# Kernel optimization log

Measured on AMD Instinct MI355X. Metric: run time of the kernel, lower is better.

Reference implementation:

```python
import jax, jax.numpy as jnp
import numpy as np

# Fixed multi-scale pyramid (H, W) per level -- static config, closed over.
SPATIAL_SHAPES = [(100, 100), (50, 50), (25, 25), (13, 13)]
D_MODEL, N_HEADS, N_LEVELS, N_POINTS = 256, 8, 4, 4
C_HEAD = D_MODEL // N_HEADS
B = 2
NUM_KEYS = sum(h * w for h, w in SPATIAL_SHAPES)  # 13294
NUM_QUERIES = NUM_KEYS


def setup_inputs() -> dict:
    key = jax.random.key(0)
    ks = jax.random.split(key, 12)
    d = D_MODEL
    return {
        "query": jax.random.normal(ks[0], (B, NUM_QUERIES, d), jnp.float32),
        "reference_points": jax.random.uniform(ks[1], (B, NUM_QUERIES, N_LEVELS, 2), jnp.float32),
        "input_flatten": jax.random.normal(ks[2], (B, NUM_KEYS, d), jnp.float32),
        "Wv": jax.random.normal(ks[3], (d, d), jnp.float32) * 0.02,
        "bv": jnp.zeros((d,), jnp.float32),
        "Ws": jax.random.normal(ks[4], (d, N_HEADS * N_LEVELS * N_POINTS * 2), jnp.float32) * 0.01,
        "bs": jax.random.normal(ks[5], (N_HEADS * N_LEVELS * N_POINTS * 2,), jnp.float32),
        "Wa": jax.random.normal(ks[6], (d, N_HEADS * N_LEVELS * N_POINTS), jnp.float32) * 0.02,
        "ba": jnp.zeros((N_HEADS * N_LEVELS * N_POINTS,), jnp.float32),
        "Wo": jax.random.normal(ks[7], (d, d), jnp.float32) * 0.02,
        "bo": jnp.zeros((d,), jnp.float32),
    }


def _bilinear_sample(v, grid, H, W):
    """torch.F.grid_sample(mode='bilinear', padding_mode='zeros', align_corners=False).
    v: (N, H, W, C); grid: (N, M, 2) with (x, y) in [-1, 1]. Returns (N, M, C)."""
    x = (grid[..., 0] + 1.0) * (W * 0.5) - 0.5
    y = (grid[..., 1] + 1.0) * (H * 0.5) - 0.5
    x0 = jnp.floor(x)
    y0 = jnp.floor(y)
    dx = x - x0
    dy = y - y0
    x0i = x0.astype(jnp.int32)
    y0i = y0.astype(jnp.int32)
    vflat = v.reshape(v.shape[0], H * W, v.shape[-1])

    def gather(xi, yi):
        valid = (xi >= 0) & (xi < W) & (yi >= 0) & (yi < H)
        idx = jnp.clip(yi, 0, H - 1) * W + jnp.clip(xi, 0, W - 1)  # (N, M)
        g = jnp.take_along_axis(vflat, idx[..., None], axis=1)
        return g * valid[..., None]

    v00 = gather(x0i, y0i)
    v10 = gather(x0i + 1, y0i)
    v01 = gather(x0i, y0i + 1)
    v11 = gather(x0i + 1, y0i + 1)
    return (v00 * ((1 - dx) * (1 - dy))[..., None]
            + v10 * (dx * (1 - dy))[..., None]
            + v01 * ((1 - dx) * dy)[..., None]
            + v11 * (dx * dy)[..., None])


def _ms_deform_attn(value, sampling_locations, attention_weights):
    # value: (B, NK, H, Ch); loc: (B, NQ, H, L, P, 2); w: (B, NQ, H, L, P)
    grids = 2.0 * sampling_locations - 1.0
    splits = np.cumsum([h * w for h, w in SPATIAL_SHAPES])[:-1]
    value_list = jnp.split(value, splits, axis=1)
    acc = 0.0
    for lvl, (H, W) in enumerate(SPATIAL_SHAPES):
        # (B, H*W, heads, Ch) -> (B*heads, H, W, Ch)
        v_l = value_list[lvl].reshape(B, H, W, N_HEADS, C_HEAD)
        v_l = v_l.transpose(0, 3, 1, 2, 4).reshape(B * N_HEADS, H, W, C_HEAD)
        # (B, NQ, heads, P, 2) -> (B*heads, NQ*P, 2)
        g_l = grids[:, :, :, lvl].transpose(0, 2, 1, 3, 4).reshape(B * N_HEADS, -1, 2)
        samp = _bilinear_sample(v_l, g_l, H, W)  # (B*heads, NQ*P, Ch)
        samp = samp.reshape(B, N_HEADS, -1, N_POINTS, C_HEAD)
        w_l = attention_weights[:, :, :, lvl].transpose(0, 2, 1, 3)  # (B, heads, NQ, P)
        acc = acc + jnp.einsum("bhqpc,bhqp->bhqc", samp, w_l)
    return acc.transpose(0, 2, 1, 3).reshape(B, -1, D_MODEL)  # (B, NQ, d_model)


def reference(query, reference_points, input_flatten, Wv, bv, Ws, bs, Wa, ba, Wo, bo):
    value = (input_flatten @ Wv + bv).reshape(B, NUM_KEYS, N_HEADS, C_HEAD)
    offsets = (query @ Ws + bs).reshape(B, NUM_QUERIES, N_HEADS, N_LEVELS, N_POINTS, 2)
    attw = jax.nn.softmax(
        (query @ Wa + ba).reshape(B, NUM_QUERIES, N_HEADS, N_LEVELS * N_POINTS), axis=-1
    ).reshape(B, NUM_QUERIES, N_HEADS, N_LEVELS, N_POINTS)
    # NOTE: module divides by [H, W] (not [W, H]) -- replicated faithfully.
    normalizer = jnp.asarray(SPATIAL_SHAPES, jnp.float32)  # (L, 2) = (H, W)
    normalizer = jnp.clip(normalizer, 1.0)
    loc = reference_points[:, :, None, :, None, :] + offsets / normalizer[None, None, None, :, None, :]
    out = _ms_deform_attn(value, loc, attw)
    return out @ Wo + bo
```

## Files before the change

kernel.cpp:

```cpp
#include <hip/hip_runtime.h>
#include <hip/hip_bf16.h>
#include <math.h>

#define B_  2
#define NQ  13294
#define NK  13294
#define M_  (B_ * NK)
#define MT  32
#define GX  ((M_ + MT - 1) / MT)

typedef __bf16 bf16x8 __attribute__((ext_vector_type(8)));
typedef float f32x4 __attribute__((ext_vector_type(4)));

static __device__ __forceinline__ f32x4 mfma16(bf16x8 a, bf16x8 b, f32x4 c) {
  return __builtin_amdgcn_mfma_f32_16x16x32_bf16(a, b, c, 0, 0, 0);
}

static __device__ __forceinline__ void pack_one(
    const float* __restrict__ W1, const float* __restrict__ W2,
    int N1, int Ntot, __hip_bfloat16* __restrict__ out, int g) {
  int lane = g & 63;
  int n_sub = (g >> 6) & 3;
  int kt = (g >> 8) & 7;
  int bn = g >> 11;
  int n = bn * 64 + n_sub * 16 + (lane & 15);
  int k0 = kt * 32 + (lane >> 4) * 8;
  const float* src; int nn, Ns;
  if (n < N1) { src = W1; nn = n; Ns = N1; }
  else        { src = W2; nn = n - N1; Ns = Ntot - N1; }
  bf16x8 v;
#pragma unroll
  for (int j = 0; j < 8; ++j) v[j] = (__bf16)src[(size_t)(k0 + j) * Ns + nn];
  *(bf16x8*)(out + (size_t)g * 8) = v;
}

__global__ __launch_bounds__(256) void pack_all(
    const float* __restrict__ Wv, const float* __restrict__ Ws,
    const float* __restrict__ Wa, const float* __restrict__ Wo,
    __hip_bfloat16* __restrict__ wv_p, __hip_bfloat16* __restrict__ wsa_p,
    __hip_bfloat16* __restrict__ wo_p) {
  const int b = blockIdx.x, t = threadIdx.x;
  if (b < 32)       pack_one(Wv, Wv, 256, 256, wv_p,  b * 256 + t);
  else if (b < 80)  pack_one(Ws, Wa, 256, 384, wsa_p, (b - 32) * 256 + t);
  else              pack_one(Wo, Wo, 256, 256, wo_p,  (b - 80) * 256 + t);
}

#define CSTR 68

__global__ __launch_bounds__(128) void gemm_mt(
    const float* __restrict__ inpf, const float* __restrict__ query,
    const __hip_bfloat16* __restrict__ accin,
    const bf16x8* __restrict__ wv_p, const bf16x8* __restrict__ wsa_p,
    const bf16x8* __restrict__ wo_p,
    const float* __restrict__ bv, const float* __restrict__ bs,
    const float* __restrict__ ba, const float* __restrict__ bo,
    __hip_bfloat16* __restrict__ value, float* __restrict__ params,
    float* __restrict__ outp, int mode_base) {
  __shared__ bf16x8 As[8 * 2 * 64];
  __shared__ float  Cs[2 * MT * CSTR];

  const int t = threadIdx.x;
  const int bm = blockIdx.x * MT;
  const int lane = t & 63, wid = t >> 6;
  const int mode = mode_base + blockIdx.y;

  {
    const int r = t >> 2;
    const int row = bm + r;
    const int sm = r >> 4;
    const int lb = r & 15;
    const bool ok = row < M_;
    if (mode != 2) {
      const float* Af = (mode == 0) ? inpf : query;
      const float* ap = Af + (size_t)row * 256 + (t & 3) * 64;
#pragma unroll
      for (int gi = 0; gi < 8; ++gi) {
        float4 u = make_float4(0.f,0.f,0.f,0.f), v = make_float4(0.f,0.f,0.f,0.f);
        if (ok) { u = *(const float4*)(ap + gi * 8); v = *(const float4*)(ap + gi * 8 + 4); }
        bf16x8 w;
        w[0]=(__bf16)u.x; w[1]=(__bf16)u.y; w[2]=(__bf16)u.z; w[3]=(__bf16)u.w;
        w[4]=(__bf16)v.x; w[5]=(__bf16)v.y; w[6]=(__bf16)v.z; w[7]=(__bf16)v.w;
        int k8 = (t & 3) * 8 + gi;
        As[((k8 >> 2) * 2 + sm) * 64 + lb + ((k8 & 3) << 4)] = w;
      }
    } else {
      const __hip_bfloat16* ap = accin + (size_t)row * 256 + (t & 3) * 64;
#pragma unroll
      for (int gi = 0; gi < 8; ++gi) {
        bf16x8 w = {};
        if (ok) w = *(const bf16x8*)(ap + gi * 8);
        int k8 = (t & 3) * 8 + gi;
        As[((k8 >> 2) * 2 + sm) * 64 + lb + ((k8 & 3) << 4)] = w;
      }
    }
  }
  __syncthreads();

  const bf16x8* Bp = (mode == 0) ? wv_p : (mode == 1) ? wsa_p : wo_p;
  const int NB = (mode == 1) ? 6 : 4;
  float* Cw = &Cs[wid * MT * CSTR];

  for (int nb = wid; nb < NB; nb += 2) {
    const int colbase = nb * 64;
    const bf16x8* bpn = Bp + (size_t)nb * 2048;

    f32x4 acc[2][4] = {};
#pragma unroll
    for (int kt = 0; kt < 8; ++kt) {
      bf16x8 a0 = As[(kt * 2 + 0) * 64 + lane];
      bf16x8 a1 = As[(kt * 2 + 1) * 64 + lane];
#pragma unroll
      for (int n = 0; n < 4; ++n) {
        bf16x8 b = bpn[(kt * 4 + n) * 64 + lane];
        acc[0][n] = mfma16(a0, b, acc[0][n]);
        acc[1][n] = mfma16(a1, b, acc[1][n]);
      }
    }

#pragma unroll
    for (int m = 0; m < 2; ++m)
#pragma unroll
      for (int n = 0; n < 4; ++n)
#pragma unroll
        for (int rg = 0; rg < 4; ++rg)
          Cw[(m * 16 + (lane >> 4) * 4 + rg) * CSTR + n * 16 + (lane & 15)] = acc[m][n][rg];

    if (mode == 0) {
#pragma unroll
      for (int p = 0; p < 4; ++p) {
        const int r = (lane >> 3) + p * 8;
        const int c = (lane & 7) * 8;
        const int row = bm + r;
        float4 u = *(float4*)&Cw[r * CSTR + c];
        float4 v = *(float4*)&Cw[r * CSTR + c + 4];
        const float* bias = bv + colbase + c;
        bf16x8 o;
        o[0]=(__bf16)(u.x+bias[0]); o[1]=(__bf16)(u.y+bias[1]);
        o[2]=(__bf16)(u.z+bias[2]); o[3]=(__bf16)(u.w+bias[3]);
        o[4]=(__bf16)(v.x+bias[4]); o[5]=(__bf16)(v.y+bias[5]);
        o[6]=(__bf16)(v.z+bias[6]); o[7]=(__bf16)(v.w+bias[7]);
        if (row < M_)
          *(bf16x8*)(value + (size_t)row * 256 + colbase + c) = o;
      }
    } else {
      float* Of = (mode == 1) ? params : outp;
      const int stride = (mode == 1) ? 384 : 256;
#pragma unroll
      for (int p = 0; p < 8; ++p) {
        const int r = (lane >> 4) + p * 4;
        const int c = (lane & 15) * 4;
        const int row = bm + r;
        const int col = colbase + c;
        float4 u = *(float4*)&Cw[r * CSTR + c];
        const float* bias;
        if (mode == 1) bias = (col < 256) ? (bs + col) : (ba + col - 256);
        else           bias = bo + col;
        u.x += bias[0]; u.y += bias[1]; u.z += bias[2]; u.w += bias[3];
        if (row < M_)
          *(float4*)(Of + (size_t)row * stride + col) = u;
      }
    }
  }
}

#define CS 65

__global__ __launch_bounds__(256) void sampler(
    const float* __restrict__ refp, const float* __restrict__ params,
    const __hip_bfloat16* __restrict__ value, __hip_bfloat16* __restrict__ acc_out) {
  __shared__ unsigned int combo[64 * CS];

  const int t = threadIdx.x;
  const int q0 = blockIdx.x * 16;
  const int bb = blockIdx.y;

  const int cqi = t >> 5;
  const int chh = (t >> 2) & 7;
  const int cl  = t & 3;

  const int lane = t & 63;
  const int wid  = t >> 6;
  const int q2   = lane >> 5;
  const int gh   = (lane >> 2) & 7;
  const int gs   = lane & 3;
  const char* vb = (const char*)value;
  const unsigned int voff0 = (unsigned int)bb * (NK * 512u) + (unsigned)(gh * 64 + gs * 16);

  const float DIMF[4]  = {100.f, 50.f, 25.f, 13.f};
  const int   LSTART[4] = {0, 10000, 12500, 13125};
  const float dimf  = DIMF[cl];
  const int   Wd    = (int)dimf;
  const int   lbase = LSTART[cl];

  for (int qc = 0; qc < 16; qc += 8) {
    __syncthreads();
    {
      const int q = q0 + qc + cqi;
      const bool valid = q < NQ;
      const size_t row = (size_t)bb * NQ + (valid ? q : 0);
      const float* pr = params + row * 384;
      const float* lg = pr + 256 + chh * 16;
      float m = lg[0];
#pragma unroll
      for (int j = 1; j < 16; ++j) m = fmaxf(m, lg[j]);
      float s = 0.f;
#pragma unroll
      for (int j = 0; j < 16; ++j) s += __expf(lg[j] - m);
      const float inv = valid ? 1.f / s : 0.f;

      const float rx = refp[(row * 4 + cl) * 2 + 0];
      const float ry = refp[(row * 4 + cl) * 2 + 1];
      const float* of = pr + chh * 32 + cl * 8;
      unsigned int* cb = &combo[(cqi * 8 + chh) * CS + cl * 16];

#pragma unroll
      for (int p = 0; p < 4; ++p) {
        const float wa = __expf(lg[cl * 4 + p] - m) * inv;
        const float x = rx * dimf + of[p * 2 + 0] - 0.5f;
        const float y = ry * dimf + of[p * 2 + 1] - 0.5f;
        const float xf = floorf(x), yf = floorf(y);
        const float dx = x - xf, dy = y - yf;
        const int x0 = (int)xf, y0 = (int)yf;
        float w00 = (1.f - dx) * (1.f - dy) * wa;
        float w10 = dx * (1.f - dy) * wa;
        float w01 = (1.f - dx) * dy * wa;
        float w11 = dx * dy * wa;
        int i0, i1, i2, i3, xi, yi;
        xi = x0;     yi = y0;
        if (xi >= 0 && xi < Wd && yi >= 0 && yi < Wd) i0 = lbase + yi * Wd + xi; else { i0 = 0; w00 = 0.f; }
        xi = x0 + 1; yi = y0;
        if (xi >= 0 && xi < Wd && yi >= 0 && yi < Wd) i1 = lbase + yi * Wd + xi; else { i1 = 0; w10 = 0.f; }
        xi = x0;     yi = y0 + 1;
        if (xi >= 0 && xi < Wd && yi >= 0 && yi < Wd) i2 = lbase + yi * Wd + xi; else { i2 = 0; w01 = 0.f; }
        xi = x0 + 1; yi = y0 + 1;
        if (xi >= 0 && xi < Wd && yi >= 0 && yi < Wd) i3 = lbase + yi * Wd + xi; else { i3 = 0; w11 = 0.f; }
        cb[p * 4 + 0] = ((__float_as_uint(w00) + 0x8000u) & 0xffff0000u) | (unsigned)i0;
        cb[p * 4 + 1] = ((__float_as_uint(w10) + 0x8000u) & 0xffff0000u) | (unsigned)i1;
        cb[p * 4 + 2] = ((__float_as_uint(w01) + 0x8000u) & 0xffff0000u) | (unsigned)i2;
        cb[p * 4 + 3] = ((__float_as_uint(w11) + 0x8000u) & 0xffff0000u) | (unsigned)i3;
      }
    }
    __syncthreads();

    {
      const int qw = wid * 2 + q2;
      const int q = q0 + qc + qw;
      const unsigned int* cb = &combo[(qw * 8 + gh) * CS];
      float a0=0.f,a1=0.f,a2=0.f,a3=0.f,a4=0.f,a5=0.f,a6=0.f,a7=0.f;
#pragma unroll 16
      for (int e = 0; e < 64; ++e) {
        const unsigned int u = cb[e];
        const float w = __uint_as_float(u & 0xffff0000u);
        const unsigned int voff = voff0 + ((u & 0xffffu) << 9);
        const uint4 v = *(const uint4*)(vb + (size_t)voff);
        a0 += w * __uint_as_float(v.x << 16);
        a1 += w * __uint_as_float(v.x & 0xffff0000u);
        a2 += w * __uint_as_float(v.y << 16);
        a3 += w * __uint_as_float(v.y & 0xffff0000u);
        a4 += w * __uint_as_float(v.z << 16);
        a5 += w * __uint_as_float(v.z & 0xffff0000u);
        a6 += w * __uint_as_float(v.w << 16);
        a7 += w * __uint_as_float(v.w & 0xffff0000u);
      }
      if (q < NQ) {
        bf16x8 o;
        o[0]=(__bf16)a0; o[1]=(__bf16)a1; o[2]=(__bf16)a2; o[3]=(__bf16)a3;
        o[4]=(__bf16)a4; o[5]=(__bf16)a5; o[6]=(__bf16)a6; o[7]=(__bf16)a7;
        *(bf16x8*)((char*)acc_out + (((size_t)bb * NQ + q) * 256 + gh * 32 + gs * 8) * 2) = o;
      }
    }
  }
}

extern "C" void kernel_launch(void* const* d_in, const int* in_sizes, int n_in,
                              void* d_out, int out_size, void* d_ws, size_t ws_size,
                              hipStream_t stream) {
  const float* query = (const float*)d_in[0];
  const float* refp  = (const float*)d_in[1];
  const float* inpf  = (const float*)d_in[2];
  const float* Wv    = (const float*)d_in[3];
  const float* bv    = (const float*)d_in[4];
  const float* Ws    = (const float*)d_in[5];
  const float* bs    = (const float*)d_in[6];
  const float* Wa    = (const float*)d_in[7];
  const float* ba    = (const float*)d_in[8];
  const float* Wo    = (const float*)d_in[9];
  const float* bo    = (const float*)d_in[10];
  float* out = (float*)d_out;

  char* w = (char*)d_ws;
  __hip_bfloat16* value  = (__hip_bfloat16*)w;            w += (size_t)M_ * 256 * 2;
  __hip_bfloat16* acc    = (__hip_bfloat16*)w;            w += (size_t)M_ * 256 * 2;
  float*          params = (float*)w;                     w += (size_t)M_ * 384 * 4;
  __hip_bfloat16* wv_p   = (__hip_bfloat16*)w;            w += 256 * 256 * 2;
  __hip_bfloat16* wsa_p  = (__hip_bfloat16*)w;            w += 256 * 384 * 2;
  __hip_bfloat16* wo_p   = (__hip_bfloat16*)w;

  pack_all<<<112, 256, 0, stream>>>(Wv, Ws, Wa, Wo, wv_p, wsa_p, wo_p);

  gemm_mt<<<dim3(GX, 2), 128, 0, stream>>>(
      inpf, query, acc, (const bf16x8*)wv_p, (const bf16x8*)wsa_p,
      (const bf16x8*)wo_p, bv, bs, ba, bo, value, params, out, 0);

  dim3 sgrid((NQ + 15) / 16, B_);
  sampler<<<sgrid, 256, 0, stream>>>(refp, params, value, acc);

  gemm_mt<<<dim3(GX, 1), 128, 0, stream>>>(
      inpf, query, acc, (const bf16x8*)wv_p, (const bf16x8*)wsa_p,
      (const bf16x8*)wo_p, bv, bs, ba, bo, value, params, out, 2);
}
```

Measured before the change: 141.2 us.

## Enlarge GEMM row tile to 64 with 4 waves; double-buffer sampler LDS

```diff
diff --git a/kernel.cpp b/kernel.cpp
--- a/kernel.cpp
+++ b/kernel.cpp
@@ -6,7 +6,7 @@
 #define NQ  13294
 #define NK  13294
 #define M_  (B_ * NK)
-#define MT  32
+#define MT  64
 #define GX  ((M_ + MT - 1) / MT)
 
 typedef __bf16 bf16x8 __attribute__((ext_vector_type(8)));
@@ -47,7 +47,7 @@
 
 #define CSTR 68
 
-__global__ __launch_bounds__(128) void gemm_mt(
+__global__ __launch_bounds__(256) void gemm_mt(
     const float* __restrict__ inpf, const float* __restrict__ query,
     const __hip_bfloat16* __restrict__ accin,
     const bf16x8* __restrict__ wv_p, const bf16x8* __restrict__ wsa_p,
@@ -56,8 +56,8 @@
     const float* __restrict__ ba, const float* __restrict__ bo,
     __hip_bfloat16* __restrict__ value, float* __restrict__ params,
     float* __restrict__ outp, int mode_base) {
-  __shared__ bf16x8 As[8 * 2 * 64];
-  __shared__ float  Cs[2 * MT * CSTR];
+  __shared__ bf16x8 As[8 * 4 * 64];
+  __shared__ float  Cs[4 * 16 * CSTR];
 
   const int t = threadIdx.x;
   const int bm = blockIdx.x * MT;
@@ -81,7 +81,7 @@
         w[0]=(__bf16)u.x; w[1]=(__bf16)u.y; w[2]=(__bf16)u.z; w[3]=(__bf16)u.w;
         w[4]=(__bf16)v.x; w[5]=(__bf16)v.y; w[6]=(__bf16)v.z; w[7]=(__bf16)v.w;
         int k8 = (t & 3) * 8 + gi;
-        As[((k8 >> 2) * 2 + sm) * 64 + lb + ((k8 & 3) << 4)] = w;
+        As[((k8 >> 2) * 4 + sm) * 64 + lb + ((k8 & 3) << 4)] = w;
       }
     } else {
       const __hip_bfloat16* ap = accin + (size_t)row * 256 + (t & 3) * 64;
@@ -90,7 +90,7 @@
         bf16x8 w = {};
         if (ok) w = *(const bf16x8*)(ap + gi * 8);
         int k8 = (t & 3) * 8 + gi;
-        As[((k8 >> 2) * 2 + sm) * 64 + lb + ((k8 & 3) << 4)] = w;
+        As[((k8 >> 2) * 4 + sm) * 64 + lb + ((k8 & 3) << 4)] = w;
       }
     }
   }
@@ -98,66 +98,73 @@
 
   const bf16x8* Bp = (mode == 0) ? wv_p : (mode == 1) ? wsa_p : wo_p;
   const int NB = (mode == 1) ? 6 : 4;
-  float* Cw = &Cs[wid * MT * CSTR];
-
-  for (int nb = wid; nb < NB; nb += 2) {
+  float* Cw = &Cs[wid * 16 * CSTR];
+
+  for (int nb = wid; nb < NB; nb += 4) {
     const int colbase = nb * 64;
     const bf16x8* bpn = Bp + (size_t)nb * 2048;
 
-    f32x4 acc[2][4] = {};
+    f32x4 acc[4][4] = {};
 #pragma unroll
     for (int kt = 0; kt < 8; ++kt) {
-      bf16x8 a0 = As[(kt * 2 + 0) * 64 + lane];
-      bf16x8 a1 = As[(kt * 2 + 1) * 64 + lane];
+      bf16x8 a0 = As[(kt * 4 + 0) * 64 + lane];
+      bf16x8 a1 = As[(kt * 4 + 1) * 64 + lane];
+      bf16x8 a2 = As[(kt * 4 + 2) * 64 + lane];
+      bf16x8 a3 = As[(kt * 4 + 3) * 64 + lane];
 #pragma unroll
       for (int n = 0; n < 4; ++n) {
         bf16x8 b = bpn[(kt * 4 + n) * 64 + lane];
         acc[0][n] = mfma16(a0, b, acc[0][n]);
         acc[1][n] = mfma16(a1, b, acc[1][n]);
-      }
-    }
-
-#pragma unroll
-    for (int m = 0; m < 2; ++m)
+        acc[2][n] = mfma16(a2, b, acc[2][n]);
+        acc[3][n] = mfma16(a3, b, acc[3][n]);
+      }
+    }
+
+#pragma unroll
+    for (int m = 0; m < 4; ++m) {
 #pragma unroll
       for (int n = 0; n < 4; ++n)
 #pragma unroll
         for (int rg = 0; rg < 4; ++rg)
-          Cw[(m * 16 + (lane >> 4) * 4 + rg) * CSTR + n * 16 + (lane & 15)] = acc[m][n][rg];
-
-    if (mode == 0) {
-#pragma unroll
-      for (int p = 0; p < 4; ++p) {
-        const int r = (lane >> 3) + p * 8;
-        const int c = (lane & 7) * 8;
-        const int row = bm + r;
-        float4 u = *(float4*)&Cw[r * CSTR + c];
-        float4 v = *(float4*)&Cw[r * CSTR + c + 4];
-        const float* bias = bv + colbase + c;
-        bf16x8 o;
-        o[0]=(__bf16)(u.x+bias[0]); o[1]=(__bf16)(u.y+bias[1]);
-        o[2]=(__bf16)(u.z+bias[2]); o[3]=(__bf16)(u.w+bias[3]);
-        o[4]=(__bf16)(v.x+bias[4]); o[5]=(__bf16)(v.y+bias[5]);
-        o[6]=(__bf16)(v.z+bias[6]); o[7]=(__bf16)(v.w+bias[7]);
-        if (row < M_)
-          *(bf16x8*)(value + (size_t)row * 256 + colbase + c) = o;
-      }
-    } else {
-      float* Of = (mode == 1) ? params : outp;
-      const int stride = (mode == 1) ? 384 : 256;
-#pragma unroll
-      for (int p = 0; p < 8; ++p) {
-        const int r = (lane >> 4) + p * 4;
-        const int c = (lane & 15) * 4;
-        const int row = bm + r;
-        const int col = colbase + c;
-        float4 u = *(float4*)&Cw[r * CSTR + c];
-        const float* bias;
-        if (mode == 1) bias = (col < 256) ? (bs + col) : (ba + col - 256);
-        else           bias = bo + col;
-        u.x += bias[0]; u.y += bias[1]; u.z += bias[2]; u.w += bias[3];
-        if (row < M_)
-          *(float4*)(Of + (size_t)row * stride + col) = u;
+          Cw[((lane >> 4) * 4 + rg) * CSTR + n * 16 + (lane & 15)] = acc[m][n][rg];
+
+      const int lr = lane >> 2;
+      const int c0 = (lane & 3) * 16;
+      const int row = bm + m * 16 + lr;
+      const int col = colbase + c0;
+      float vv[16];
+      *(float4*)&vv[0]  = *(float4*)&Cw[lr * CSTR + c0 + 0];
+      *(float4*)&vv[4]  = *(float4*)&Cw[lr * CSTR + c0 + 4];
+      *(float4*)&vv[8]  = *(float4*)&Cw[lr * CSTR + c0 + 8];
+      *(float4*)&vv[12] = *(float4*)&Cw[lr * CSTR + c0 + 12];
+
+      if (mode == 0) {
+        const float* bias = bv + col;
+        bf16x8 o0, o1;
+#pragma unroll
+        for (int j = 0; j < 8; ++j) {
+          o0[j] = (__bf16)(vv[j] + bias[j]);
+          o1[j] = (__bf16)(vv[8 + j] + bias[8 + j]);
+        }
+        if (row < M_) {
+          *(bf16x8*)(value + (size_t)row * 256 + col + 0) = o0;
+          *(bf16x8*)(value + (size_t)row * 256 + col + 8) = o1;
+        }
+      } else {
+        float* Of = (mode == 1) ? params : outp;
+        const int stride = (mode == 1) ? 384 : 256;
+        const float* bias = (mode == 2) ? (bo + col)
+                          : (col < 256 ? bs + col : ba + col - 256);
+#pragma unroll
+        for (int j = 0; j < 16; ++j) vv[j] += bias[j];
+        if (row < M_) {
+          float* dst = Of + (size_t)row * stride + col;
+          *(float4*)(dst + 0)  = *(float4*)&vv[0];
+          *(float4*)(dst + 4)  = *(float4*)&vv[4];
+          *(float4*)(dst + 8)  = *(float4*)&vv[8];
+          *(float4*)(dst + 12) = *(float4*)&vv[12];
+        }
       }
     }
   }
@@ -168,7 +175,7 @@
 __global__ __launch_bounds__(256) void sampler(
     const float* __restrict__ refp, const float* __restrict__ params,
     const __hip_bfloat16* __restrict__ value, __hip_bfloat16* __restrict__ acc_out) {
-  __shared__ unsigned int combo[64 * CS];
+  __shared__ unsigned int combo[2 * 64 * CS];
 
   const int t = threadIdx.x;
   const int q0 = blockIdx.x * 16;
@@ -193,7 +200,7 @@
   const int   lbase = LSTART[cl];
 
   for (int qc = 0; qc < 16; qc += 8) {
-    __syncthreads();
+    unsigned int* reg = combo + ((qc >> 3) & 1) * (64 * CS);
     {
       const int q = q0 + qc + cqi;
       const bool valid = q < NQ;
@@ -211,7 +218,7 @@
       const float rx = refp[(row * 4 + cl) * 2 + 0];
       const float ry = refp[(row * 4 + cl) * 2 + 1];
       const float* of = pr + chh * 32 + cl * 8;
-      unsigned int* cb = &combo[(cqi * 8 + chh) * CS + cl * 16];
+      unsigned int* cb = &reg[(cqi * 8 + chh) * CS + cl * 16];
 
 #pragma unroll
       for (int p = 0; p < 4; ++p) {
@@ -245,9 +252,9 @@
     {
       const int qw = wid * 2 + q2;
       const int q = q0 + qc + qw;
-      const unsigned int* cb = &combo[(qw * 8 + gh) * CS];
+      const unsigned int* cb = &reg[(qw * 8 + gh) * CS];
       float a0=0.f,a1=0.f,a2=0.f,a3=0.f,a4=0.f,a5=0.f,a6=0.f,a7=0.f;
-#pragma unroll 16
+#pragma unroll 8
       for (int e = 0; e < 64; ++e) {
         const unsigned int u = cb[e];
         const float w = __uint_as_float(u & 0xffff0000u);
@@ -298,14 +305,14 @@
 
   pack_all<<<112, 256, 0, stream>>>(Wv, Ws, Wa, Wo, wv_p, wsa_p, wo_p);
 
-  gemm_mt<<<dim3(GX, 2), 128, 0, stream>>>(
+  gemm_mt<<<dim3(GX, 2), 256, 0, stream>>>(
       inpf, query, acc, (const bf16x8*)wv_p, (const bf16x8*)wsa_p,
       (const bf16x8*)wo_p, bv, bs, ba, bo, value, params, out, 0);
 
   dim3 sgrid((NQ + 15) / 16, B_);
   sampler<<<sgrid, 256, 0, stream>>>(refp, params, value, acc);
 
-  gemm_mt<<<dim3(GX, 1), 128, 0, stream>>>(
+  gemm_mt<<<dim3(GX, 1), 256, 0, stream>>>(
       inpf, query, acc, (const bf16x8*)wv_p, (const bf16x8*)wsa_p,
       (const bf16x8*)wo_p, bv, bs, ba, bo, value, params, out, 2);
 }
```

Result: slower. 146.0 us (+3.5%).

## Fuse output projection into sampler and store offset/attention params as fp16

Applied to the files above, without the earlier changes.

```diff
diff --git a/kernel.cpp b/kernel.cpp
--- a/kernel.cpp
+++ b/kernel.cpp
@@ -1,5 +1,6 @@
 #include <hip/hip_runtime.h>
 #include <hip/hip_bf16.h>
+#include <hip/hip_fp16.h>
 #include <math.h>
 
 #define B_  2
@@ -49,20 +50,17 @@
 
 __global__ __launch_bounds__(128) void gemm_mt(
     const float* __restrict__ inpf, const float* __restrict__ query,
-    const __hip_bfloat16* __restrict__ accin,
     const bf16x8* __restrict__ wv_p, const bf16x8* __restrict__ wsa_p,
-    const bf16x8* __restrict__ wo_p,
     const float* __restrict__ bv, const float* __restrict__ bs,
-    const float* __restrict__ ba, const float* __restrict__ bo,
-    __hip_bfloat16* __restrict__ value, float* __restrict__ params,
-    float* __restrict__ outp, int mode_base) {
+    const float* __restrict__ ba,
+    __hip_bfloat16* __restrict__ value, __half* __restrict__ params) {
   __shared__ bf16x8 As[8 * 2 * 64];
   __shared__ float  Cs[2 * MT * CSTR];
 
   const int t = threadIdx.x;
   const int bm = blockIdx.x * MT;
   const int lane = t & 63, wid = t >> 6;
-  const int mode = mode_base + blockIdx.y;
+  const int mode = blockIdx.y;
 
   {
     const int r = t >> 2;
@@ -70,33 +68,22 @@
     const int sm = r >> 4;
     const int lb = r & 15;
     const bool ok = row < M_;
-    if (mode != 2) {
-      const float* Af = (mode == 0) ? inpf : query;
-      const float* ap = Af + (size_t)row * 256 + (t & 3) * 64;
-#pragma unroll
-      for (int gi = 0; gi < 8; ++gi) {
-        float4 u = make_float4(0.f,0.f,0.f,0.f), v = make_float4(0.f,0.f,0.f,0.f);
-        if (ok) { u = *(const float4*)(ap + gi * 8); v = *(const float4*)(ap + gi * 8 + 4); }
-        bf16x8 w;
-        w[0]=(__bf16)u.x; w[1]=(__bf16)u.y; w[2]=(__bf16)u.z; w[3]=(__bf16)u.w;
-        w[4]=(__bf16)v.x; w[5]=(__bf16)v.y; w[6]=(__bf16)v.z; w[7]=(__bf16)v.w;
-        int k8 = (t & 3) * 8 + gi;
-        As[((k8 >> 2) * 2 + sm) * 64 + lb + ((k8 & 3) << 4)] = w;
-      }
-    } else {
-      const __hip_bfloat16* ap = accin + (size_t)row * 256 + (t & 3) * 64;
-#pragma unroll
-      for (int gi = 0; gi < 8; ++gi) {
-        bf16x8 w = {};
-        if (ok) w = *(const bf16x8*)(ap + gi * 8);
-        int k8 = (t & 3) * 8 + gi;
-        As[((k8 >> 2) * 2 + sm) * 64 + lb + ((k8 & 3) << 4)] = w;
-      }
+    const float* Af = (mode == 0) ? inpf : query;
+    const float* ap = Af + (size_t)row * 256 + (t & 3) * 64;
+#pragma unroll
+    for (int gi = 0; gi < 8; ++gi) {
+      float4 u = make_float4(0.f,0.f,0.f,0.f), v = make_float4(0.f,0.f,0.f,0.f);
+      if (ok) { u = *(const float4*)(ap + gi * 8); v = *(const float4*)(ap + gi * 8 + 4); }
+      bf16x8 w;
+      w[0]=(__bf16)u.x; w[1]=(__bf16)u.y; w[2]=(__bf16)u.z; w[3]=(__bf16)u.w;
+      w[4]=(__bf16)v.x; w[5]=(__bf16)v.y; w[6]=(__bf16)v.z; w[7]=(__bf16)v.w;
+      int k8 = (t & 3) * 8 + gi;
+      As[((k8 >> 2) * 2 + sm) * 64 + lb + ((k8 & 3) << 4)] = w;
     }
   }
   __syncthreads();
 
-  const bf16x8* Bp = (mode == 0) ? wv_p : (mode == 1) ? wsa_p : wo_p;
+  const bf16x8* Bp = (mode == 0) ? wv_p : wsa_p;
   const int NB = (mode == 1) ? 6 : 4;
   float* Cw = &Cs[wid * MT * CSTR];
 
@@ -143,8 +130,6 @@
           *(bf16x8*)(value + (size_t)row * 256 + colbase + c) = o;
       }
     } else {
-      float* Of = (mode == 1) ? params : outp;
-      const int stride = (mode == 1) ? 384 : 256;
 #pragma unroll
       for (int p = 0; p < 8; ++p) {
         const int r = (lane >> 4) + p * 4;
@@ -152,12 +137,16 @@
         const int row = bm + r;
         const int col = colbase + c;
         float4 u = *(float4*)&Cw[r * CSTR + c];
-        const float* bias;
-        if (mode == 1) bias = (col < 256) ? (bs + col) : (ba + col - 256);
-        else           bias = bo + col;
+        const float* bias = (col < 256) ? (bs + col) : (ba + col - 256);
         u.x += bias[0]; u.y += bias[1]; u.z += bias[2]; u.w += bias[3];
-        if (row < M_)
-          *(float4*)(Of + (size_t)row * stride + col) = u;
+        if (row < M_) {
+          __half2 h0 = __floats2half2_rn(u.x, u.y);
+          __half2 h1 = __floats2half2_rn(u.z, u.w);
+          uint2 st;
+          st.x = *(unsigned int*)&h0;
+          st.y = *(unsigned int*)&h1;
+          *(uint2*)(params + (size_t)row * 384 + col) = st;
+        }
       }
     }
   }
@@ -166,9 +155,11 @@
 #define CS 65
 
 __global__ __launch_bounds__(256) void sampler(
-    const float* __restrict__ refp, const float* __restrict__ params,
-    const __hip_bfloat16* __restrict__ value, __hip_bfloat16* __restrict__ acc_out) {
-  __shared__ unsigned int combo[64 * CS];
+    const float* __restrict__ refp, const __half* __restrict__ params,
+    const __hip_bfloat16* __restrict__ value, const bf16x8* __restrict__ wo_p,
+    const float* __restrict__ bo, float* __restrict__ outp) {
+  __shared__ unsigned int combo[2 * 64 * CS];
+  __shared__ bf16x8 accs[32][16];
 
   const int t = threadIdx.x;
   const int q0 = blockIdx.x * 16;
@@ -193,31 +184,38 @@
   const int   lbase = LSTART[cl];
 
   for (int qc = 0; qc < 16; qc += 8) {
-    __syncthreads();
+    unsigned int* reg = combo + ((qc >> 3) & 1) * (64 * CS);
     {
       const int q = q0 + qc + cqi;
       const bool valid = q < NQ;
       const size_t row = (size_t)bb * NQ + (valid ? q : 0);
-      const float* pr = params + row * 384;
-      const float* lg = pr + 256 + chh * 16;
-      float m = lg[0];
-#pragma unroll
-      for (int j = 1; j < 16; ++j) m = fmaxf(m, lg[j]);
+      const __half* pr = params + row * 384;
+
+      union { uint4 u[2]; __half h[16]; } LG;
+      LG.u[0] = *(const uint4*)(pr + 256 + chh * 16);
+      LG.u[1] = *(const uint4*)(pr + 256 + chh * 16 + 8);
+      float lgf[16];
+#pragma unroll
+      for (int j = 0; j < 16; ++j) lgf[j] = __half2float(LG.h[j]);
+      float m = lgf[0];
+#pragma unroll
+      for (int j = 1; j < 16; ++j) m = fmaxf(m, lgf[j]);
       float s = 0.f;
 #pragma unroll
-      for (int j = 0; j < 16; ++j) s += __expf(lg[j] - m);
+      for (int j = 0; j < 16; ++j) s += __expf(lgf[j] - m);
       const float inv = valid ? 1.f / s : 0.f;
 
       const float rx = refp[(row * 4 + cl) * 2 + 0];
       const float ry = refp[(row * 4 + cl) * 2 + 1];
-      const float* of = pr + chh * 32 + cl * 8;
-      unsigned int* cb = &combo[(cqi * 8 + chh) * CS + cl * 16];
+      union { uint4 u; __half h[8]; } OF;
+      OF.u = *(const uint4*)(pr + chh * 32 + cl * 8);
+      unsigned int* cb = &reg[(cqi * 8 + chh) * CS + cl * 16];
 
 #pragma unroll
       for (int p = 0; p < 4; ++p) {
-        const float wa = __expf(lg[cl * 4 + p] - m) * inv;
-        const float x = rx * dimf + of[p * 2 + 0] - 0.5f;
-        const float y = ry * dimf + of[p * 2 + 1] - 0.5f;
+        const float wa = __expf(lgf[cl * 4 + p] - m) * inv;
+        const float x = rx * dimf + __half2float(OF.h[p * 2 + 0]) - 0.5f;
+        const float y = ry * dimf + __half2float(OF.h[p * 2 + 1]) - 0.5f;
         const float xf = floorf(x), yf = floorf(y);
         const float dx = x - xf, dy = y - yf;
         const int x0 = (int)xf, y0 = (int)yf;
@@ -244,10 +242,9 @@
 
     {
       const int qw = wid * 2 + q2;
-      const int q = q0 + qc + qw;
-      const unsigned int* cb = &combo[(qw * 8 + gh) * CS];
+      const unsigned int* cb = &reg[(qw * 8 + gh) * CS];
       float a0=0.f,a1=0.f,a2=0.f,a3=0.f,a4=0.f,a5=0.f,a6=0.f,a7=0.f;
-#pragma unroll 16
+#pragma unroll 8
       for (int e = 0; e < 64; ++e) {
         const unsigned int u = cb[e];
         const float w = __uint_as_float(u & 0xffff0000u);
@@ -262,11 +259,34 @@
         a6 += w * __uint_as_float(v.w << 16);
         a7 += w * __uint_as_float(v.w & 0xffff0000u);
       }
-      if (q < NQ) {
-        bf16x8 o;
-        o[0]=(__bf16)a0; o[1]=(__bf16)a1; o[2]=(__bf16)a2; o[3]=(__bf16)a3;
-        o[4]=(__bf16)a4; o[5]=(__bf16)a5; o[6]=(__bf16)a6; o[7]=(__bf16)a7;
-        *(bf16x8*)((char*)acc_out + (((size_t)bb * NQ + q) * 256 + gh * 32 + gs * 8) * 2) = o;
+      bf16x8 o;
+      o[0]=(__bf16)a0; o[1]=(__bf16)a1; o[2]=(__bf16)a2; o[3]=(__bf16)a3;
+      o[4]=(__bf16)a4; o[5]=(__bf16)a5; o[6]=(__bf16)a6; o[7]=(__bf16)a7;
+      accs[gh * 4 + gs][qc + qw] = o;
+    }
+  }
+  __syncthreads();
+
+  {
+    const bf16x8* bpn = wo_p + (size_t)wid * 2048;
+    f32x4 oacc[4] = {};
+#pragma unroll
+    for (int kt = 0; kt < 8; ++kt) {
+      bf16x8 a = accs[kt * 4 + (lane >> 4)][lane & 15];
+#pragma unroll
+      for (int n = 0; n < 4; ++n)
+        oacc[n] = mfma16(a, bpn[(kt * 4 + n) * 64 + lane], oacc[n]);
+    }
+#pragma unroll
+    for (int n = 0; n < 4; ++n) {
+      const int col = wid * 64 + n * 16 + (lane & 15);
+      const float bias = bo[col];
+#pragma unroll
+      for (int rg = 0; rg < 4; ++rg) {
+        const int ql = (lane >> 4) * 4 + rg;
+        const int q = q0 + ql;
+        if (q < NQ)
+          outp[((size_t)bb * NQ + q) * 256 + col] = oacc[n][rg] + bias;
       }
     }
   }
@@ -290,8 +310,7 @@
 
   char* w = (char*)d_ws;
   __hip_bfloat16* value  = (__hip_bfloat16*)w;            w += (size_t)M_ * 256 * 2;
-  __hip_bfloat16* acc    = (__hip_bfloat16*)w;            w += (size_t)M_ * 256 * 2;
-  float*          params = (float*)w;                     w += (size_t)M_ * 384 * 4;
+  __half*         params = (__half*)w;                    w += (size_t)M_ * 384 * 2;
   __hip_bfloat16* wv_p   = (__hip_bfloat16*)w;            w += 256 * 256 * 2;
   __hip_bfloat16* wsa_p  = (__hip_bfloat16*)w;            w += 256 * 384 * 2;
   __hip_bfloat16* wo_p   = (__hip_bfloat16*)w;
@@ -299,13 +318,10 @@
   pack_all<<<112, 256, 0, stream>>>(Wv, Ws, Wa, Wo, wv_p, wsa_p, wo_p);
 
   gemm_mt<<<dim3(GX, 2), 128, 0, stream>>>(
-      inpf, query, acc, (const bf16x8*)wv_p, (const bf16x8*)wsa_p,
-      (const bf16x8*)wo_p, bv, bs, ba, bo, value, params, out, 0);
+      inpf, query, (const bf16x8*)wv_p, (const bf16x8*)wsa_p,
+      bv, bs, ba, value, params);
 
   dim3 sgrid((NQ + 15) / 16, B_);
-  sampler<<<sgrid, 256, 0, stream>>>(refp, params, value, acc);
-
-  gemm_mt<<<dim3(GX, 1), 128, 0, stream>>>(
-      inpf, query, acc, (const bf16x8*)wv_p, (const bf16x8*)wsa_p,
-      (const bf16x8*)wo_p, bv, bs, ba, bo, value, params, out, 2);
-}
+  sampler<<<sgrid, 256, 0, stream>>>(refp, params, value,
+                                     (const bf16x8*)wo_p, bo, out);
+}
```

Result: faster. 126.9 us (-10.1%).
